# Kernel optimization log

Hardware: AMD Instinct MI355X
Metric: run time of the kernel (lower is better)

## Reference

```python
import jax, jax.numpy as jnp
import numpy as np

EMBED_DIM = 128
N_NODES = 100000
N_PAIRS = 500000


def setup_inputs() -> dict:
    key = jax.random.key(0)
    k_h, k_p, k1, k2, k3, kb1, kb2, kb3 = jax.random.split(key, 8)
    h = jax.random.normal(k_h, (N_NODES, EMBED_DIM), dtype=jnp.float32)
    pairs = jax.random.randint(k_p, (N_PAIRS, 2), 0, N_NODES, dtype=jnp.int64)
    d_in = EMBED_DIM * 4  # 512
    # Kaiming-uniform-ish init scales
    W1 = jax.random.normal(k1, (d_in, 128), dtype=jnp.float32) / np.sqrt(d_in)
    b1 = jnp.zeros((128,), dtype=jnp.float32)
    W2 = jax.random.normal(k2, (128, 64), dtype=jnp.float32) / np.sqrt(128)
    b2 = jnp.zeros((64,), dtype=jnp.float32)
    W3 = jax.random.normal(k3, (64, 1), dtype=jnp.float32) / np.sqrt(64)
    b3 = jnp.zeros((1,), dtype=jnp.float32)
    return {"h": h, "pairs": pairs, "W1": W1, "b1": b1, "W2": W2, "b2": b2, "W3": W3, "b3": b3}


def reference(h, pairs, W1, b1, W2, b2, W3, b3):
    # Gather source/target node embeddings
    hs = h[pairs[:, 0]]  # [P, D]
    ht = h[pairs[:, 1]]  # [P, D]
    feat = jnp.concatenate([hs, ht, hs * ht, jnp.abs(hs - ht)], axis=1)  # [P, 4D]
    # 3-layer MLP (dropout is identity in eval mode)
    x = jax.nn.relu(feat @ W1 + b1)
    x = jax.nn.relu(x @ W2 + b2)
    logit = (x @ W3 + b3)[:, 0]  # [P]
    return logit
```

## Files before the change

kernel.cpp:

```cpp
#include <hip/hip_runtime.h>
#include <math.h>

#define EMBED 128
#define NPB 128

typedef short s16x8 __attribute__((ext_vector_type(8)));
typedef float f32x16 __attribute__((ext_vector_type(16)));
#define MF(a, b, c) __builtin_amdgcn_mfma_f32_32x32x16_bf16((a), (b), (c), 0, 0, 0)

__device__ __forceinline__ unsigned short f2bf(float f) {
    unsigned u = __float_as_uint(f);
    return (unsigned short)((u + 0x7FFF + ((u >> 16) & 1)) >> 16);
}
__device__ __forceinline__ float bf2f(unsigned short h) {
    return __uint_as_float(((unsigned)h) << 16);
}

__global__ void detect_kernel(const unsigned int* __restrict__ pairs,
                              int* __restrict__ flag) {
    unsigned v = 0;
    int lane = threadIdx.x;
#pragma unroll
    for (int i = 0; i < 8; ++i) v |= pairs[2 * (lane * 8 + i) + 1];
    unsigned long long b = __ballot(v != 0);
    if (lane == 0) *flag = (b != 0ULL) ? 1 : 0;
}

__global__ __launch_bounds__(256) void setup_w_kernel(
    const float* __restrict__ W1, const float* __restrict__ W2,
    unsigned short* __restrict__ W1Fh, unsigned short* __restrict__ W1Fl,
    unsigned short* __restrict__ W2Fh, unsigned short* __restrict__ W2Fl)
{
    int gid = blockIdx.x * 256 + threadIdx.x;
    if (gid < 8192) {
        int f = gid;
        int jt = f >> 11, r = f & 2047;
        int gk = r >> 6, lane = r & 63;
        int j = jt * 32 + (lane & 31);
        int kb = gk * 16 + (lane >> 5) * 8;
#pragma unroll
        for (int e = 0; e < 8; ++e) {
            float w = W1[(size_t)(kb + e) * 128 + j];
            unsigned short hb = f2bf(w);
            unsigned short lb = f2bf(w - bf2f(hb));
            W1Fh[(size_t)f * 8 + e] = hb;
            W1Fl[(size_t)f * 8 + e] = lb;
        }
    } else if (gid < 9216) {
        int f = gid - 8192;
        int nt = f >> 9, r = f & 511;
        int gk = r >> 6, lane = r & 63;
        int i = nt * 32 + (lane & 31);
        int kb = gk * 16 + (lane >> 5) * 8;
#pragma unroll
        for (int e = 0; e < 8; ++e) {
            float w = W2[(size_t)(kb + e) * 64 + i];
            unsigned short hb = f2bf(w);
            unsigned short lb = f2bf(w - bf2f(hb));
            W2Fh[(size_t)f * 8 + e] = hb;
            W2Fl[(size_t)f * 8 + e] = lb;
        }
    }
}

template<int MODE>
__device__ __forceinline__ void make_frag(
    const float* __restrict__ hsL, const float* __restrict__ htL,
    int row, int dcol, s16x8& aH, s16x8& aL)
{
    float av[8], bv[8];
    if (MODE != 1) {
        float4 a0 = *(const float4*)(hsL + row * 68 + dcol);
        float4 a1 = *(const float4*)(hsL + row * 68 + dcol + 4);
        av[0] = a0.x; av[1] = a0.y; av[2] = a0.z; av[3] = a0.w;
        av[4] = a1.x; av[5] = a1.y; av[6] = a1.z; av[7] = a1.w;
    }
    if (MODE != 0) {
        float4 b0 = *(const float4*)(htL + row * 68 + dcol);
        float4 b1 = *(const float4*)(htL + row * 68 + dcol + 4);
        bv[0] = b0.x; bv[1] = b0.y; bv[2] = b0.z; bv[3] = b0.w;
        bv[4] = b1.x; bv[5] = b1.y; bv[6] = b1.z; bv[7] = b1.w;
    }
#pragma unroll
    for (int e = 0; e < 8; ++e) {
        float v;
        if (MODE == 0)      v = av[e];
        else if (MODE == 1) v = bv[e];
        else if (MODE == 2) v = av[e] * bv[e];
        else                v = fabsf(av[e] - bv[e]);
        unsigned short hb = f2bf(v);
        unsigned short lb = f2bf(v - bf2f(hb));
        aH[e] = (short)hb; aL[e] = (short)lb;
    }
}

template<int MODE>
__device__ __forceinline__ void l1_phase(
    const float* __restrict__ hsL, const float* __restrict__ htL,
    const unsigned short* __restrict__ W1Fh, const unsigned short* __restrict__ W1Fl,
    int pA, int ghalf, int lane, int gkbase,
    f32x16& ac0, f32x16& ac1, f32x16& ac2, f32x16& ac3)
{
#pragma unroll
    for (int ks = 0; ks < 4; ++ks) {
        int dcol = ks * 16 + ghalf * 8;
        s16x8 aH, aL;
        make_frag<MODE>(hsL, htL, pA, dcol, aH, aL);
        int gk = gkbase + ks;
        size_t bi0 = ((size_t)(0 * 32 + gk) * 64 + lane) * 8;
        size_t bi1 = ((size_t)(1 * 32 + gk) * 64 + lane) * 8;
        size_t bi2 = ((size_t)(2 * 32 + gk) * 64 + lane) * 8;
        size_t bi3 = ((size_t)(3 * 32 + gk) * 64 + lane) * 8;
        s16x8 bH0 = *(const s16x8*)&W1Fh[bi0];
        s16x8 bL0 = *(const s16x8*)&W1Fl[bi0];
        s16x8 bH1 = *(const s16x8*)&W1Fh[bi1];
        s16x8 bL1 = *(const s16x8*)&W1Fl[bi1];
        s16x8 bH2 = *(const s16x8*)&W1Fh[bi2];
        s16x8 bL2 = *(const s16x8*)&W1Fl[bi2];
        s16x8 bH3 = *(const s16x8*)&W1Fh[bi3];
        s16x8 bL3 = *(const s16x8*)&W1Fl[bi3];
        ac0 = MF(aH, bH0, ac0); ac0 = MF(aH, bL0, ac0); ac0 = MF(aL, bH0, ac0);
        ac1 = MF(aH, bH1, ac1); ac1 = MF(aH, bL1, ac1); ac1 = MF(aL, bH1, ac1);
        ac2 = MF(aH, bH2, ac2); ac2 = MF(aH, bL2, ac2); ac2 = MF(aL, bH2, ac2);
        ac3 = MF(aH, bH3, ac3); ac3 = MF(aH, bL3, ac3); ac3 = MF(aL, bH3, ac3);
    }
}

__global__ __launch_bounds__(256, 2) void pair_mfma_kernel(
    const float* __restrict__ h,
    const int* __restrict__ pairs,
    const int* __restrict__ flag,
    const unsigned short* __restrict__ W1Fh, const unsigned short* __restrict__ W1Fl,
    const unsigned short* __restrict__ W2Fh, const unsigned short* __restrict__ W2Fl,
    const float* __restrict__ b1, const float* __restrict__ b2,
    const float* __restrict__ W3, const float* __restrict__ b3,
    float* __restrict__ out, int npairs)
{
    __shared__ __align__(16) char buf[69632];
    __shared__ int sArr[NPB], tArr[NPB];
    float* hsL = (float*)buf;
    float* htL = (float*)(buf + 34816);
    unsigned short* fbH = (unsigned short*)buf;
    unsigned short* fbL = (unsigned short*)(buf + 34816);

    int tid  = threadIdx.x;
    int lane = tid & 63;
    int w    = tid >> 6;
    int pb   = blockIdx.x * NPB;

    if (tid < NPB) {
        int p = pb + tid; if (p >= npairs) p = npairs - 1;
        int s, t;
        if (*flag == 0) { s = pairs[4 * p]; t = pairs[4 * p + 2]; }
        else            { s = pairs[2 * p]; t = pairs[2 * p + 1]; }
        sArr[tid] = s; tArr[tid] = t;
    }
    __syncthreads();

    int r  = tid & 127;
    int nd = tid >> 7;
    const float* gsrc = h + (size_t)(nd ? tArr[r] : sArr[r]) * EMBED;
    float* ldst = (nd ? htL : hsL) + r * 68;

    int ghalf = lane >> 5;
    int pA = w * 32 + (lane & 31);

    float bj0 = b1[  0 + (lane & 31)];
    float bj1 = b1[ 32 + (lane & 31)];
    float bj2 = b1[ 64 + (lane & 31)];
    float bj3 = b1[ 96 + (lane & 31)];
    f32x16 ac0, ac1, ac2, ac3;
#pragma unroll
    for (int rg = 0; rg < 16; ++rg) { ac0[rg] = bj0; ac1[rg] = bj1; ac2[rg] = bj2; ac3[rg] = bj3; }

    {
        const float4* s4 = (const float4*)gsrc;
        float4* d4 = (float4*)ldst;
#pragma unroll
        for (int q = 0; q < 16; ++q) d4[q] = s4[q];
    }
    __syncthreads();
    l1_phase<0>(hsL, htL, W1Fh, W1Fl, pA, ghalf, lane,  0, ac0, ac1, ac2, ac3);
    l1_phase<1>(hsL, htL, W1Fh, W1Fl, pA, ghalf, lane,  8, ac0, ac1, ac2, ac3);
    l1_phase<2>(hsL, htL, W1Fh, W1Fl, pA, ghalf, lane, 16, ac0, ac1, ac2, ac3);
    l1_phase<3>(hsL, htL, W1Fh, W1Fl, pA, ghalf, lane, 24, ac0, ac1, ac2, ac3);
    __syncthreads();

    {
        const float4* s4 = (const float4*)(gsrc + 64);
        float4* d4 = (float4*)ldst;
#pragma unroll
        for (int q = 0; q < 16; ++q) d4[q] = s4[q];
    }
    __syncthreads();
    l1_phase<0>(hsL, htL, W1Fh, W1Fl, pA, ghalf, lane,  4, ac0, ac1, ac2, ac3);
    l1_phase<1>(hsL, htL, W1Fh, W1Fl, pA, ghalf, lane, 12, ac0, ac1, ac2, ac3);
    l1_phase<2>(hsL, htL, W1Fh, W1Fl, pA, ghalf, lane, 20, ac0, ac1, ac2, ac3);
    l1_phase<3>(hsL, htL, W1Fh, W1Fl, pA, ghalf, lane, 28, ac0, ac1, ac2, ac3);
    __syncthreads();

#define X1WR(ACC, jt) do {                                                   \
    int jbase = (jt) * 32 + (lane & 31);                                     \
    int gj = jbase >> 3, jrem = jbase & 7;                                   \
    _Pragma("unroll")                                                        \
    for (int reg = 0; reg < 16; ++reg) {                                     \
        int pr = w * 32 + (reg & 3) + 8 * (reg >> 2) + 4 * ghalf;            \
        float x = fmaxf(ACC[reg], 0.0f);                                     \
        unsigned short hb = f2bf(x);                                         \
        unsigned short lb = f2bf(x - bf2f(hb));                              \
        int idx = pr * 136 + ((gj ^ ((pr >> 3) & 7)) * 8) + jrem;            \
        fbH[idx] = hb; fbL[idx] = lb;                                        \
    } } while (0)

    X1WR(ac0, 0); X1WR(ac1, 1); X1WR(ac2, 2); X1WR(ac3, 3);
#undef X1WR
    __syncthreads();

    int pB0 = 64 * (w & 1) + (lane & 31), pB1 = pB0 + 32;
    int oB0base = pB0 * 136, oB1base = pB1 * 136;
    int sb0 = (pB0 >> 3) & 7, sb1 = (pB1 >> 3) & 7;
    int nt = w >> 1;
    int iCol = nt * 32 + (lane & 31);

    float b2v = b2[iCol];
    f32x16 c20, c21;
#pragma unroll
    for (int rg = 0; rg < 16; ++rg) { c20[rg] = b2v; c21[rg] = b2v; }

#pragma unroll
    for (int ks = 0; ks < 8; ++ks) {
        int g = ks * 2 + ghalf;
        int o0 = oB0base + (g ^ sb0) * 8;
        int o1 = oB1base + (g ^ sb1) * 8;
        s16x8 aH0 = *(const s16x8*)&fbH[o0];
        s16x8 aL0 = *(const s16x8*)&fbL[o0];
        s16x8 aH1 = *(const s16x8*)&fbH[o1];
        s16x8 aL1 = *(const s16x8*)&fbL[o1];
        size_t bi = ((size_t)(nt * 8 + ks) * 64 + lane) * 8;
        s16x8 bH = *(const s16x8*)&W2Fh[bi];
        s16x8 bL = *(const s16x8*)&W2Fl[bi];
        c20 = MF(aH0, bH, c20); c20 = MF(aH0, bL, c20); c20 = MF(aL0, bH, c20);
        c21 = MF(aH1, bH, c21); c21 = MF(aH1, bL, c21); c21 = MF(aL1, bH, c21);
    }
    __syncthreads();

    float* red = (float*)buf;
    {
        float w3v = W3[iCol];
#pragma unroll
        for (int reg = 0; reg < 16; ++reg) {
            int pr = 64 * (w & 1) + (reg & 3) + 8 * (reg >> 2) + 4 * ghalf;
            red[pr * 68 + iCol] = fmaxf(c20[reg], 0.0f) * w3v;
        }
#pragma unroll
        for (int reg = 0; reg < 16; ++reg) {
            int pr = 64 * (w & 1) + 32 + (reg & 3) + 8 * (reg >> 2) + 4 * ghalf;
            red[pr * 68 + iCol] = fmaxf(c21[reg], 0.0f) * w3v;
        }
    }
    __syncthreads();

    if (tid < NPB) {
        int p = pb + tid;
        if (p < npairs) {
            const float4* r4 = (const float4*)(red + tid * 68);
            float s = 0.0f;
#pragma unroll
            for (int q = 0; q < 16; ++q) {
                float4 v = r4[q];
                s += v.x + v.y + v.z + v.w;
            }
            out[p] = s + b3[0];
        }
    }
}

__global__ __launch_bounds__(256) void mlp_kernel(
    const float* __restrict__ h,
    const int* __restrict__ pairs,
    const int* __restrict__ flag,
    const float* __restrict__ W1, const float* __restrict__ b1,
    const float* __restrict__ W2, const float* __restrict__ b2,
    const float* __restrict__ W3, const float* __restrict__ b3,
    float* __restrict__ out, int npairs)
{
    int p = blockIdx.x * 256 + threadIdx.x;
    if (p >= npairs) return;
    int s, t;
    if (*flag == 0) { s = pairs[4 * p]; t = pairs[4 * p + 2]; }
    else            { s = pairs[2 * p]; t = pairs[2 * p + 1]; }
    const float4* hs4 = (const float4*)(h + (size_t)s * EMBED);
    const float4* ht4 = (const float4*)(h + (size_t)t * EMBED);
    float acc[128];
#pragma unroll
    for (int j = 0; j < 128; ++j) acc[j] = b1[j];
#pragma unroll 1
    for (int d4 = 0; d4 < EMBED / 4; ++d4) {
        float4 a = hs4[d4]; float4 b = ht4[d4];
        float av[4] = {a.x, a.y, a.z, a.w};
        float bv[4] = {b.x, b.y, b.z, b.w};
#pragma unroll
        for (int dd = 0; dd < 4; ++dd) {
            int k = d4 * 4 + dd;
            float f0 = av[dd], f1 = bv[dd];
            float f2 = f0 * f1, f3 = fabsf(f0 - f1);
            const float* w0 = W1 + (size_t)k * 128;
            const float* w1r = w0 + 128 * 128;
            const float* w2r = w0 + 256 * 128;
            const float* w3r = w0 + 384 * 128;
#pragma unroll
            for (int j = 0; j < 128; ++j) {
                float v0 = acc[j];
                v0 = fmaf(f0, w0[j], v0); v0 = fmaf(f1, w1r[j], v0);
                v0 = fmaf(f2, w2r[j], v0); v0 = fmaf(f3, w3r[j], v0);
                acc[j] = v0;
            }
        }
    }
#pragma unroll
    for (int j = 0; j < 128; ++j) acc[j] = fmaxf(acc[j], 0.0f);
    float x2[64];
#pragma unroll
    for (int j = 0; j < 64; ++j) x2[j] = b2[j];
#pragma unroll
    for (int k = 0; k < 128; ++k) {
        float xv = acc[k];
#pragma unroll
        for (int j = 0; j < 64; ++j)
            x2[j] = fmaf(xv, W2[(size_t)k * 64 + j], x2[j]);
    }
    float lg = b3[0];
#pragma unroll
    for (int k = 0; k < 64; ++k)
        lg = fmaf(fmaxf(x2[k], 0.0f), W3[k], lg);
    out[p] = lg;
}

extern "C" void kernel_launch(void* const* d_in, const int* in_sizes, int n_in,
                              void* d_out, int out_size, void* d_ws, size_t ws_size,
                              hipStream_t stream) {
    const float* h   = (const float*)d_in[0];
    const int* pairs = (const int*)d_in[1];
    const float* W1  = (const float*)d_in[2];
    const float* b1  = (const float*)d_in[3];
    const float* W2  = (const float*)d_in[4];
    const float* b2  = (const float*)d_in[5];
    const float* W3  = (const float*)d_in[6];
    const float* b3  = (const float*)d_in[7];
    float* out = (float*)d_out;

    int npairs = out_size;

    int* flag = (int*)d_ws;
    unsigned short* base = (unsigned short*)((char*)d_ws + 16);
    unsigned short* W1Fh = base;
    unsigned short* W1Fl = base + 65536;
    unsigned short* W2Fh = base + 131072;
    unsigned short* W2Fl = base + 139264;
    size_t need = 16 + (size_t)(65536 * 2 + 8192 * 2) * sizeof(unsigned short);

    detect_kernel<<<1, 64, 0, stream>>>((const unsigned int*)pairs, flag);

    if (ws_size >= need) {
        setup_w_kernel<<<36, 256, 0, stream>>>(W1, W2, W1Fh, W1Fl, W2Fh, W2Fl);
        pair_mfma_kernel<<<(npairs + NPB - 1) / NPB, 256, 0, stream>>>(
            h, pairs, flag, W1Fh, W1Fl, W2Fh, W2Fl, b1, b2, W3, b3, out, npairs);
    } else {
        mlp_kernel<<<(npairs + 255) / 256, 256, 0, stream>>>(
            h, pairs, flag, W1, b1, W2, b2, W3, b3, out, npairs);
    }
}
```

Baseline: 286.3 us.

## Precompute per-node layer-1 projections for hs and ht terms in a node table

```diff
diff --git a/kernel.cpp b/kernel.cpp
--- a/kernel.cpp
+++ b/kernel.cpp
@@ -26,18 +26,119 @@
     if (lane == 0) *flag = (b != 0ULL) ? 1 : 0;
 }
 
+__global__ __launch_bounds__(256) void node_pre_kernel(
+    const float* __restrict__ h, const float* __restrict__ W1,
+    const float* __restrict__ b1, float* __restrict__ tab, int n_nodes)
+{
+    __shared__ float Wab[16 * 260];
+    __shared__ float Fh[16 * 64];
+
+    int tid = threadIdx.x;
+    int pg  = tid & 15;
+    int cg  = tid >> 4;
+    int nb  = blockIdx.x * 64;
+
+    const float4* hP = nullptr;
+    if (tid < 64) {
+        int n = nb + tid; if (n >= n_nodes) n = n_nodes - 1;
+        hP = (const float4*)(h + (size_t)n * EMBED);
+    }
+
+    float acc[4][16];
+#pragma unroll
+    for (int a = 0; a < 4; ++a)
+#pragma unroll
+        for (int b = 0; b < 16; ++b) acc[a][b] = 0.0f;
+
+    int wr   = tid >> 4;
+    int wseg = tid & 15;
+
+#pragma unroll 1
+    for (int c = 0; c < 8; ++c) {
+        {
+            const float* src = (wseg < 8)
+                ? (W1 + (size_t)(c * 16 + wr) * 128 + wseg * 16)
+                : (W1 + (size_t)(128 + c * 16 + wr) * 128 + (wseg - 8) * 16);
+            float* dst = Wab + wr * 260 + ((wseg < 8) ? wseg * 16
+                                                      : 128 + (wseg - 8) * 16);
+            const float4* s4 = (const float4*)src;
+            float4* d4 = (float4*)dst;
+#pragma unroll
+            for (int q = 0; q < 4; ++q) d4[q] = s4[q];
+        }
+        if (tid < 64) {
+#pragma unroll
+            for (int q = 0; q < 4; ++q) {
+                float4 v = hP[c * 4 + q];
+                Fh[(q * 4 + 0) * 64 + tid] = v.x;
+                Fh[(q * 4 + 1) * 64 + tid] = v.y;
+                Fh[(q * 4 + 2) * 64 + tid] = v.z;
+                Fh[(q * 4 + 3) * 64 + tid] = v.w;
+            }
+        }
+        __syncthreads();
+#pragma unroll 4
+        for (int k = 0; k < 16; ++k) {
+            float4 f = *(const float4*)(Fh + k * 64 + pg * 4);
+            float fa[4] = {f.x, f.y, f.z, f.w};
+            const float4* wrow = (const float4*)(Wab + k * 260 + cg * 16);
+#pragma unroll
+            for (int q = 0; q < 4; ++q) {
+                float4 wv = wrow[q];
+                float wa[4] = {wv.x, wv.y, wv.z, wv.w};
+#pragma unroll
+                for (int a = 0; a < 4; ++a)
+#pragma unroll
+                    for (int b = 0; b < 4; ++b)
+                        acc[a][q * 4 + b] = fmaf(fa[a], wa[b], acc[a][q * 4 + b]);
+            }
+        }
+        __syncthreads();
+    }
+
+    float bias[16];
+    if (cg < 8) {
+        const float4* b4 = (const float4*)(b1 + cg * 16);
+#pragma unroll
+        for (int q = 0; q < 4; ++q) {
+            float4 v = b4[q];
+            bias[q * 4 + 0] = v.x; bias[q * 4 + 1] = v.y;
+            bias[q * 4 + 2] = v.z; bias[q * 4 + 3] = v.w;
+        }
+    } else {
+#pragma unroll
+        for (int b = 0; b < 16; ++b) bias[b] = 0.0f;
+    }
+#pragma unroll
+    for (int a = 0; a < 4; ++a) {
+        int n = nb + pg * 4 + a;
+        if (n < n_nodes) {
+            int row = (cg < 8) ? 2 * n : 2 * n + 1;
+            int col = (cg < 8) ? cg * 16 : (cg - 8) * 16;
+            float4* dst = (float4*)(tab + (size_t)row * 128 + col);
+#pragma unroll
+            for (int q = 0; q < 4; ++q)
+                dst[q] = make_float4(acc[a][q * 4 + 0] + bias[q * 4 + 0],
+                                     acc[a][q * 4 + 1] + bias[q * 4 + 1],
+                                     acc[a][q * 4 + 2] + bias[q * 4 + 2],
+                                     acc[a][q * 4 + 3] + bias[q * 4 + 3]);
+        }
+    }
+}
+
 __global__ __launch_bounds__(256) void setup_w_kernel(
     const float* __restrict__ W1, const float* __restrict__ W2,
     unsigned short* __restrict__ W1Fh, unsigned short* __restrict__ W1Fl,
     unsigned short* __restrict__ W2Fh, unsigned short* __restrict__ W2Fl)
 {
     int gid = blockIdx.x * 256 + threadIdx.x;
-    if (gid < 8192) {
+    if (gid < 4096) {
         int f = gid;
-        int jt = f >> 11, r = f & 2047;
+        int jt = f >> 10, r = f & 1023;
         int gk = r >> 6, lane = r & 63;
         int j = jt * 32 + (lane & 31);
-        int kb = gk * 16 + (lane >> 5) * 8;
+        int kb = ((gk < 8) ? (256 + gk * 16) : (384 + (gk - 8) * 16))
+                 + (lane >> 5) * 8;
 #pragma unroll
         for (int e = 0; e < 8; ++e) {
             float w = W1[(size_t)(kb + e) * 128 + j];
@@ -46,8 +147,8 @@
             W1Fh[(size_t)f * 8 + e] = hb;
             W1Fl[(size_t)f * 8 + e] = lb;
         }
-    } else if (gid < 9216) {
-        int f = gid - 8192;
+    } else if (gid < 5120) {
+        int f = gid - 4096;
         int nt = f >> 9, r = f & 511;
         int gk = r >> 6, lane = r & 63;
         int i = nt * 32 + (lane & 31);
@@ -69,13 +170,13 @@
     int row, int dcol, s16x8& aH, s16x8& aL)
 {
     float av[8], bv[8];
-    if (MODE != 1) {
+    {
         float4 a0 = *(const float4*)(hsL + row * 68 + dcol);
         float4 a1 = *(const float4*)(hsL + row * 68 + dcol + 4);
         av[0] = a0.x; av[1] = a0.y; av[2] = a0.z; av[3] = a0.w;
         av[4] = a1.x; av[5] = a1.y; av[6] = a1.z; av[7] = a1.w;
     }
-    if (MODE != 0) {
+    {
         float4 b0 = *(const float4*)(htL + row * 68 + dcol);
         float4 b1 = *(const float4*)(htL + row * 68 + dcol + 4);
         bv[0] = b0.x; bv[1] = b0.y; bv[2] = b0.z; bv[3] = b0.w;
@@ -83,11 +184,7 @@
     }
 #pragma unroll
     for (int e = 0; e < 8; ++e) {
-        float v;
-        if (MODE == 0)      v = av[e];
-        else if (MODE == 1) v = bv[e];
-        else if (MODE == 2) v = av[e] * bv[e];
-        else                v = fabsf(av[e] - bv[e]);
+        float v = (MODE == 2) ? (av[e] * bv[e]) : fabsf(av[e] - bv[e]);
         unsigned short hb = f2bf(v);
         unsigned short lb = f2bf(v - bf2f(hb));
         aH[e] = (short)hb; aL[e] = (short)lb;
@@ -107,10 +204,10 @@
         s16x8 aH, aL;
         make_frag<MODE>(hsL, htL, pA, dcol, aH, aL);
         int gk = gkbase + ks;
-        size_t bi0 = ((size_t)(0 * 32 + gk) * 64 + lane) * 8;
-        size_t bi1 = ((size_t)(1 * 32 + gk) * 64 + lane) * 8;
-        size_t bi2 = ((size_t)(2 * 32 + gk) * 64 + lane) * 8;
-        size_t bi3 = ((size_t)(3 * 32 + gk) * 64 + lane) * 8;
+        size_t bi0 = ((size_t)(0 * 16 + gk) * 64 + lane) * 8;
+        size_t bi1 = ((size_t)(1 * 16 + gk) * 64 + lane) * 8;
+        size_t bi2 = ((size_t)(2 * 16 + gk) * 64 + lane) * 8;
+        size_t bi3 = ((size_t)(3 * 16 + gk) * 64 + lane) * 8;
         s16x8 bH0 = *(const s16x8*)&W1Fh[bi0];
         s16x8 bL0 = *(const s16x8*)&W1Fl[bi0];
         s16x8 bH1 = *(const s16x8*)&W1Fh[bi1];
@@ -130,9 +227,10 @@
     const float* __restrict__ h,
     const int* __restrict__ pairs,
     const int* __restrict__ flag,
+    const float* __restrict__ tab,
     const unsigned short* __restrict__ W1Fh, const unsigned short* __restrict__ W1Fl,
     const unsigned short* __restrict__ W2Fh, const unsigned short* __restrict__ W2Fl,
-    const float* __restrict__ b1, const float* __restrict__ b2,
+    const float* __restrict__ b2,
     const float* __restrict__ W3, const float* __restrict__ b3,
     float* __restrict__ out, int npairs)
 {
@@ -165,13 +263,9 @@
     int ghalf = lane >> 5;
     int pA = w * 32 + (lane & 31);
 
-    float bj0 = b1[  0 + (lane & 31)];
-    float bj1 = b1[ 32 + (lane & 31)];
-    float bj2 = b1[ 64 + (lane & 31)];
-    float bj3 = b1[ 96 + (lane & 31)];
     f32x16 ac0, ac1, ac2, ac3;
 #pragma unroll
-    for (int rg = 0; rg < 16; ++rg) { ac0[rg] = bj0; ac1[rg] = bj1; ac2[rg] = bj2; ac3[rg] = bj3; }
+    for (int rg = 0; rg < 16; ++rg) { ac0[rg] = 0.f; ac1[rg] = 0.f; ac2[rg] = 0.f; ac3[rg] = 0.f; }
 
     {
         const float4* s4 = (const float4*)gsrc;
@@ -180,10 +274,8 @@
         for (int q = 0; q < 16; ++q) d4[q] = s4[q];
     }
     __syncthreads();
-    l1_phase<0>(hsL, htL, W1Fh, W1Fl, pA, ghalf, lane,  0, ac0, ac1, ac2, ac3);
-    l1_phase<1>(hsL, htL, W1Fh, W1Fl, pA, ghalf, lane,  8, ac0, ac1, ac2, ac3);
-    l1_phase<2>(hsL, htL, W1Fh, W1Fl, pA, ghalf, lane, 16, ac0, ac1, ac2, ac3);
-    l1_phase<3>(hsL, htL, W1Fh, W1Fl, pA, ghalf, lane, 24, ac0, ac1, ac2, ac3);
+    l1_phase<2>(hsL, htL, W1Fh, W1Fl, pA, ghalf, lane,  0, ac0, ac1, ac2, ac3);
+    l1_phase<3>(hsL, htL, W1Fh, W1Fl, pA, ghalf, lane,  8, ac0, ac1, ac2, ac3);
     __syncthreads();
 
     {
@@ -193,27 +285,31 @@
         for (int q = 0; q < 16; ++q) d4[q] = s4[q];
     }
     __syncthreads();
-    l1_phase<0>(hsL, htL, W1Fh, W1Fl, pA, ghalf, lane,  4, ac0, ac1, ac2, ac3);
-    l1_phase<1>(hsL, htL, W1Fh, W1Fl, pA, ghalf, lane, 12, ac0, ac1, ac2, ac3);
-    l1_phase<2>(hsL, htL, W1Fh, W1Fl, pA, ghalf, lane, 20, ac0, ac1, ac2, ac3);
-    l1_phase<3>(hsL, htL, W1Fh, W1Fl, pA, ghalf, lane, 28, ac0, ac1, ac2, ac3);
-    __syncthreads();
-
-#define X1WR(ACC, jt) do {                                                   \
-    int jbase = (jt) * 32 + (lane & 31);                                     \
-    int gj = jbase >> 3, jrem = jbase & 7;                                   \
-    _Pragma("unroll")                                                        \
-    for (int reg = 0; reg < 16; ++reg) {                                     \
-        int pr = w * 32 + (reg & 3) + 8 * (reg >> 2) + 4 * ghalf;            \
-        float x = fmaxf(ACC[reg], 0.0f);                                     \
-        unsigned short hb = f2bf(x);                                         \
-        unsigned short lb = f2bf(x - bf2f(hb));                              \
-        int idx = pr * 136 + ((gj ^ ((pr >> 3) & 7)) * 8) + jrem;            \
-        fbH[idx] = hb; fbL[idx] = lb;                                        \
-    } } while (0)
-
-    X1WR(ac0, 0); X1WR(ac1, 1); X1WR(ac2, 2); X1WR(ac3, 3);
-#undef X1WR
+    l1_phase<2>(hsL, htL, W1Fh, W1Fl, pA, ghalf, lane,  4, ac0, ac1, ac2, ac3);
+    l1_phase<3>(hsL, htL, W1Fh, W1Fl, pA, ghalf, lane, 12, ac0, ac1, ac2, ac3);
+    __syncthreads();
+
+    {
+        int l31 = lane & 31;
+#pragma unroll
+        for (int reg = 0; reg < 16; ++reg) {
+            int pr = w * 32 + (reg & 3) + 8 * (reg >> 2) + 4 * ghalf;
+            const float* Arow = tab + (size_t)(2 * sArr[pr]) * EMBED;
+            const float* Brow = tab + (size_t)(2 * tArr[pr] + 1) * EMBED;
+            int swz = (pr >> 3) & 7;
+#define ONE(ACC, jt) { \
+            int jbase = (jt) * 32 + l31; \
+            float x = ACC[reg] + Arow[jbase] + Brow[jbase]; \
+            x = fmaxf(x, 0.0f); \
+            unsigned short hb = f2bf(x); \
+            unsigned short lb = f2bf(x - bf2f(hb)); \
+            int gj = jbase >> 3, jrem = jbase & 7; \
+            int idx = pr * 136 + ((gj ^ swz) * 8) + jrem; \
+            fbH[idx] = hb; fbL[idx] = lb; }
+            ONE(ac0, 0) ONE(ac1, 1) ONE(ac2, 2) ONE(ac3, 3)
+#undef ONE
+        }
+    }
     __syncthreads();
 
     int pB0 = 64 * (w & 1) + (lane & 31), pB1 = pB0 + 32;
@@ -349,22 +445,27 @@
     const float* b3  = (const float*)d_in[7];
     float* out = (float*)d_out;
 
-    int npairs = out_size;
-
-    int* flag = (int*)d_ws;
-    unsigned short* base = (unsigned short*)((char*)d_ws + 16);
+    int npairs  = out_size;
+    int n_nodes = in_sizes[0] / EMBED;
+
+    size_t tabBytes = (size_t)n_nodes * 2 * EMBED * sizeof(float);
+    int*   flag = (int*)d_ws;
+    float* tab  = (float*)((char*)d_ws + 16);
+    unsigned short* base = (unsigned short*)((char*)d_ws + 16 + tabBytes);
     unsigned short* W1Fh = base;
-    unsigned short* W1Fl = base + 65536;
-    unsigned short* W2Fh = base + 131072;
-    unsigned short* W2Fl = base + 139264;
-    size_t need = 16 + (size_t)(65536 * 2 + 8192 * 2) * sizeof(unsigned short);
+    unsigned short* W1Fl = base + 32768;
+    unsigned short* W2Fh = base + 65536;
+    unsigned short* W2Fl = base + 73728;
+    size_t need = 16 + tabBytes + (size_t)81920 * sizeof(unsigned short);
 
     detect_kernel<<<1, 64, 0, stream>>>((const unsigned int*)pairs, flag);
 
     if (ws_size >= need) {
-        setup_w_kernel<<<36, 256, 0, stream>>>(W1, W2, W1Fh, W1Fl, W2Fh, W2Fl);
+        node_pre_kernel<<<(n_nodes + 63) / 64, 256, 0, stream>>>(
+            h, W1, b1, tab, n_nodes);
+        setup_w_kernel<<<20, 256, 0, stream>>>(W1, W2, W1Fh, W1Fl, W2Fh, W2Fl);
         pair_mfma_kernel<<<(npairs + NPB - 1) / NPB, 256, 0, stream>>>(
-            h, pairs, flag, W1Fh, W1Fl, W2Fh, W2Fl, b1, b2, W3, b3, out, npairs);
+            h, pairs, flag, tab, W1Fh, W1Fl, W2Fh, W2Fl, b2, W3, b3, out, npairs);
     } else {
         mlp_kernel<<<(npairs + 255) / 256, 256, 0, stream>>>(
             h, pairs, flag, W1, b1, W2, b2, W3, b3, out, npairs);
```

Result: slower. 370.1 us (+29.3%).

## Load gathered embeddings directly into registers instead of staging through LDS

Applied to the files above, without the earlier changes.

```diff
diff --git a/kernel.cpp b/kernel.cpp
--- a/kernel.cpp
+++ b/kernel.cpp
@@ -64,20 +64,15 @@
 }
 
 template<int MODE>
-__device__ __forceinline__ void make_frag(
-    const float* __restrict__ hsL, const float* __restrict__ htL,
-    int row, int dcol, s16x8& aH, s16x8& aL)
+__device__ __forceinline__ void make_frag_r(
+    const float4* ha, const float4* hb, int ks, s16x8& aH, s16x8& aL)
 {
     float av[8], bv[8];
-    if (MODE != 1) {
-        float4 a0 = *(const float4*)(hsL + row * 68 + dcol);
-        float4 a1 = *(const float4*)(hsL + row * 68 + dcol + 4);
+    {
+        float4 a0 = ha[2 * ks], a1 = ha[2 * ks + 1];
         av[0] = a0.x; av[1] = a0.y; av[2] = a0.z; av[3] = a0.w;
         av[4] = a1.x; av[5] = a1.y; av[6] = a1.z; av[7] = a1.w;
-    }
-    if (MODE != 0) {
-        float4 b0 = *(const float4*)(htL + row * 68 + dcol);
-        float4 b1 = *(const float4*)(htL + row * 68 + dcol + 4);
+        float4 b0 = hb[2 * ks], b1 = hb[2 * ks + 1];
         bv[0] = b0.x; bv[1] = b0.y; bv[2] = b0.z; bv[3] = b0.w;
         bv[4] = b1.x; bv[5] = b1.y; bv[6] = b1.z; bv[7] = b1.w;
     }
@@ -88,24 +83,23 @@
         else if (MODE == 1) v = bv[e];
         else if (MODE == 2) v = av[e] * bv[e];
         else                v = fabsf(av[e] - bv[e]);
-        unsigned short hb = f2bf(v);
-        unsigned short lb = f2bf(v - bf2f(hb));
-        aH[e] = (short)hb; aL[e] = (short)lb;
+        unsigned short hbit = f2bf(v);
+        unsigned short lbit = f2bf(v - bf2f(hbit));
+        aH[e] = (short)hbit; aL[e] = (short)lbit;
     }
 }
 
 template<int MODE>
-__device__ __forceinline__ void l1_phase(
-    const float* __restrict__ hsL, const float* __restrict__ htL,
+__device__ __forceinline__ void l1_phase_r(
+    const float4* ha, const float4* hb,
     const unsigned short* __restrict__ W1Fh, const unsigned short* __restrict__ W1Fl,
-    int pA, int ghalf, int lane, int gkbase,
+    int lane, int gkbase,
     f32x16& ac0, f32x16& ac1, f32x16& ac2, f32x16& ac3)
 {
 #pragma unroll
     for (int ks = 0; ks < 4; ++ks) {
-        int dcol = ks * 16 + ghalf * 8;
         s16x8 aH, aL;
-        make_frag<MODE>(hsL, htL, pA, dcol, aH, aL);
+        make_frag_r<MODE>(ha, hb, ks, aH, aL);
         int gk = gkbase + ks;
         size_t bi0 = ((size_t)(0 * 32 + gk) * 64 + lane) * 8;
         size_t bi1 = ((size_t)(1 * 32 + gk) * 64 + lane) * 8;
@@ -126,7 +120,7 @@
     }
 }
 
-__global__ __launch_bounds__(256, 2) void pair_mfma_kernel(
+__global__ __launch_bounds__(256) void pair_mfma_kernel(
     const float* __restrict__ h,
     const int* __restrict__ pairs,
     const int* __restrict__ flag,
@@ -137,9 +131,6 @@
     float* __restrict__ out, int npairs)
 {
     __shared__ __align__(16) char buf[69632];
-    __shared__ int sArr[NPB], tArr[NPB];
-    float* hsL = (float*)buf;
-    float* htL = (float*)(buf + 34816);
     unsigned short* fbH = (unsigned short*)buf;
     unsigned short* fbL = (unsigned short*)(buf + 34816);
 
@@ -148,22 +139,15 @@
     int w    = tid >> 6;
     int pb   = blockIdx.x * NPB;
 
-    if (tid < NPB) {
-        int p = pb + tid; if (p >= npairs) p = npairs - 1;
-        int s, t;
-        if (*flag == 0) { s = pairs[4 * p]; t = pairs[4 * p + 2]; }
-        else            { s = pairs[2 * p]; t = pairs[2 * p + 1]; }
-        sArr[tid] = s; tArr[tid] = t;
-    }
-    __syncthreads();
-
-    int r  = tid & 127;
-    int nd = tid >> 7;
-    const float* gsrc = h + (size_t)(nd ? tArr[r] : sArr[r]) * EMBED;
-    float* ldst = (nd ? htL : hsL) + r * 68;
-
     int ghalf = lane >> 5;
     int pA = w * 32 + (lane & 31);
+
+    int p = pb + pA; if (p >= npairs) p = npairs - 1;
+    int s, t;
+    if (*flag == 0) { s = pairs[4 * p]; t = pairs[4 * p + 2]; }
+    else            { s = pairs[2 * p]; t = pairs[2 * p + 1]; }
+    const float4* hsP = (const float4*)(h + (size_t)s * EMBED);
+    const float4* htP = (const float4*)(h + (size_t)t * EMBED);
 
     float bj0 = b1[  0 + (lane & 31)];
     float bj1 = b1[ 32 + (lane & 31)];
@@ -173,31 +157,31 @@
 #pragma unroll
     for (int rg = 0; rg < 16; ++rg) { ac0[rg] = bj0; ac1[rg] = bj1; ac2[rg] = bj2; ac3[rg] = bj3; }
 
-    {
-        const float4* s4 = (const float4*)gsrc;
-        float4* d4 = (float4*)ldst;
-#pragma unroll
-        for (int q = 0; q < 16; ++q) d4[q] = s4[q];
-    }
-    __syncthreads();
-    l1_phase<0>(hsL, htL, W1Fh, W1Fl, pA, ghalf, lane,  0, ac0, ac1, ac2, ac3);
-    l1_phase<1>(hsL, htL, W1Fh, W1Fl, pA, ghalf, lane,  8, ac0, ac1, ac2, ac3);
-    l1_phase<2>(hsL, htL, W1Fh, W1Fl, pA, ghalf, lane, 16, ac0, ac1, ac2, ac3);
-    l1_phase<3>(hsL, htL, W1Fh, W1Fl, pA, ghalf, lane, 24, ac0, ac1, ac2, ac3);
-    __syncthreads();
-
-    {
-        const float4* s4 = (const float4*)(gsrc + 64);
-        float4* d4 = (float4*)ldst;
-#pragma unroll
-        for (int q = 0; q < 16; ++q) d4[q] = s4[q];
-    }
-    __syncthreads();
-    l1_phase<0>(hsL, htL, W1Fh, W1Fl, pA, ghalf, lane,  4, ac0, ac1, ac2, ac3);
-    l1_phase<1>(hsL, htL, W1Fh, W1Fl, pA, ghalf, lane, 12, ac0, ac1, ac2, ac3);
-    l1_phase<2>(hsL, htL, W1Fh, W1Fl, pA, ghalf, lane, 20, ac0, ac1, ac2, ac3);
-    l1_phase<3>(hsL, htL, W1Fh, W1Fl, pA, ghalf, lane, 28, ac0, ac1, ac2, ac3);
-    __syncthreads();
+    float4 ha[8], hb[8];
+
+#pragma unroll
+    for (int ks = 0; ks < 4; ++ks) {
+        ha[2 * ks]     = hsP[ks * 4 + ghalf * 2];
+        ha[2 * ks + 1] = hsP[ks * 4 + ghalf * 2 + 1];
+        hb[2 * ks]     = htP[ks * 4 + ghalf * 2];
+        hb[2 * ks + 1] = htP[ks * 4 + ghalf * 2 + 1];
+    }
+    l1_phase_r<0>(ha, hb, W1Fh, W1Fl, lane,  0, ac0, ac1, ac2, ac3);
+    l1_phase_r<1>(ha, hb, W1Fh, W1Fl, lane,  8, ac0, ac1, ac2, ac3);
+    l1_phase_r<2>(ha, hb, W1Fh, W1Fl, lane, 16, ac0, ac1, ac2, ac3);
+    l1_phase_r<3>(ha, hb, W1Fh, W1Fl, lane, 24, ac0, ac1, ac2, ac3);
+
+#pragma unroll
+    for (int ks = 0; ks < 4; ++ks) {
+        ha[2 * ks]     = hsP[16 + ks * 4 + ghalf * 2];
+        ha[2 * ks + 1] = hsP[16 + ks * 4 + ghalf * 2 + 1];
+        hb[2 * ks]     = htP[16 + ks * 4 + ghalf * 2];
+        hb[2 * ks + 1] = htP[16 + ks * 4 + ghalf * 2 + 1];
+    }
+    l1_phase_r<0>(ha, hb, W1Fh, W1Fl, lane,  4, ac0, ac1, ac2, ac3);
+    l1_phase_r<1>(ha, hb, W1Fh, W1Fl, lane, 12, ac0, ac1, ac2, ac3);
+    l1_phase_r<2>(ha, hb, W1Fh, W1Fl, lane, 20, ac0, ac1, ac2, ac3);
+    l1_phase_r<3>(ha, hb, W1Fh, W1Fl, lane, 28, ac0, ac1, ac2, ac3);
 
 #define X1WR(ACC, jt) do {                                                   \
     int jbase = (jt) * 32 + (lane & 31);                                     \
@@ -206,10 +190,10 @@
     for (int reg = 0; reg < 16; ++reg) {                                     \
         int pr = w * 32 + (reg & 3) + 8 * (reg >> 2) + 4 * ghalf;            \
         float x = fmaxf(ACC[reg], 0.0f);                                     \
-        unsigned short hb = f2bf(x);                                         \
-        unsigned short lb = f2bf(x - bf2f(hb));                              \
+        unsigned short hbit = f2bf(x);                                       \
+        unsigned short lbit = f2bf(x - bf2f(hbit));                          \
         int idx = pr * 136 + ((gj ^ ((pr >> 3) & 7)) * 8) + jrem;            \
-        fbH[idx] = hb; fbL[idx] = lb;                                        \
+        fbH[idx] = hbit; fbL[idx] = lbit;                                    \
     } } while (0)
 
     X1WR(ac0, 0); X1WR(ac1, 1); X1WR(ac2, 2); X1WR(ac3, 3);
@@ -261,16 +245,16 @@
     __syncthreads();
 
     if (tid < NPB) {
-        int p = pb + tid;
-        if (p < npairs) {
+        int po = pb + tid;
+        if (po < npairs) {
             const float4* r4 = (const float4*)(red + tid * 68);
-            float s = 0.0f;
+            float ssum = 0.0f;
 #pragma unroll
             for (int q = 0; q < 16; ++q) {
                 float4 v = r4[q];
-                s += v.x + v.y + v.z + v.w;
+                ssum += v.x + v.y + v.z + v.w;
             }
-            out[p] = s + b3[0];
+            out[po] = ssum + b3[0];
         }
     }
 }
```

New measurement: 267.6 us. -6.6%, faster.
